# Kernel optimization log

Measured on AMD Instinct MI355X. Metric: run time of the kernel, lower is better.

## Reference

```python
import jax, jax.numpy as jnp
import numpy as np

EMBED_DIM = 1024
NUM_HEAD = 16
HEAD_DIM = EMBED_DIM // NUM_HEAD
SCALE = HEAD_DIM ** -0.5
EPS = 1e-6


def setup_inputs() -> dict:
    key = jax.random.key(0)
    ks = jax.random.split(key, 8)
    B, N, K, D = 4, 2048, 2048, EMBED_DIM
    x = jax.random.normal(ks[0], (B, N, D), dtype=jnp.float32)
    ctx = jax.random.normal(ks[1], (B, K, D), dtype=jnp.float32)
    w_std = 0.02
    q_w = jax.random.normal(ks[2], (D, D), dtype=jnp.float32) * w_std  # [in, out]
    q_b = jnp.zeros((D,), dtype=jnp.float32)
    kv_w = jax.random.normal(ks[3], (D, 2 * D), dtype=jnp.float32) * w_std
    kv_b = jnp.zeros((2 * D,), dtype=jnp.float32)
    proj_w = jax.random.normal(ks[4], (D, D), dtype=jnp.float32) * w_std
    proj_b = jnp.zeros((D,), dtype=jnp.float32)
    return {"x": x, "ctx": ctx, "q_w": q_w, "q_b": q_b,
            "kv_w": kv_w, "kv_b": kv_b, "proj_w": proj_w, "proj_b": proj_b}


def rms_norm(t):
    return t * jax.lax.rsqrt(jnp.mean(t * t, axis=-1, keepdims=True) + EPS)


def reference(x, ctx, q_w, q_b, kv_w, kv_b, proj_w, proj_b):
    B, N, D = x.shape
    Kc = ctx.shape[1]
    H, Hd = NUM_HEAD, HEAD_DIM
    ctxn = rms_norm(ctx)
    q = (x @ q_w + q_b).reshape(B, N, H, Hd)                 # bnhd
    kv = (ctxn @ kv_w + kv_b).reshape(B, Kc, 2, H, Hd)
    k, v = kv[:, :, 0], kv[:, :, 1]                          # bkhd
    logits = jnp.einsum('bnhd,bkhd->bhnk', q * SCALE, k)
    logits = jnp.clip(logits, -10.0, 10.0)
    attn = jax.nn.softmax(logits, axis=-1)                   # bhnk
    out = jnp.einsum('bhnk,bkhd->bnhd', attn, v).reshape(B, N, D)
    out = out @ proj_w + proj_b
    return out, attn.mean()
```

## Files before the change

### kernel.cpp

```cpp
#include <hip/hip_runtime.h>
#include <hip/hip_bf16.h>
#include <stdint.h>


typedef __bf16 bf16_t;
typedef __bf16 bf16x8 __attribute__((ext_vector_type(8)));
typedef __bf16 bf16x4 __attribute__((ext_vector_type(4)));
typedef short  s16x4  __attribute__((ext_vector_type(4)));
typedef float  f32x4  __attribute__((ext_vector_type(4)));

#define BB 4
#define NN 2048
#define KC 2048
#define DD 1024
#define NH 16
#define HD 64
#define QSCALE 0.18033688011112042f
#define CLIP2  14.426950408889634f

__device__ __forceinline__ f32x4 mfma_16x16x32(bf16x8 a, bf16x8 b, f32x4 c) {
  return __builtin_amdgcn_mfma_f32_16x16x32_bf16(a, b, c, 0, 0, 0);
}

__device__ __forceinline__ void gl_lds16(const bf16_t* g, bf16_t* l) {
  __builtin_amdgcn_global_load_lds(
      (const __attribute__((address_space(1))) void*)g,
      (__attribute__((address_space(3))) void*)l, 16, 0, 0);
}

__global__ __launch_bounds__(256) void cvt_f32_bf16(const float* __restrict__ in,
                                                    bf16_t* __restrict__ out, int n4) {
  int i = blockIdx.x * 256 + threadIdx.x;
  if (i >= n4) return;
  float4 v = ((const float4*)in)[i];
  bf16x4 o = {(bf16_t)v.x, (bf16_t)v.y, (bf16_t)v.z, (bf16_t)v.w};
  ((bf16x4*)out)[i] = o;
}

__global__ __launch_bounds__(256) void rmsnorm_rows(const float* __restrict__ in,
                                                    bf16_t* __restrict__ out) {
  int row = blockIdx.x, tid = threadIdx.x;
  float4 v = ((const float4*)(in + (size_t)row * DD))[tid];
  float ss = v.x * v.x + v.y * v.y + v.z * v.z + v.w * v.w;
#pragma unroll
  for (int m = 1; m < 64; m <<= 1) ss += __shfl_xor(ss, m);
  __shared__ float wsum[4];
  if ((tid & 63) == 0) wsum[tid >> 6] = ss;
  __syncthreads();
  float total = wsum[0] + wsum[1] + wsum[2] + wsum[3];
  float scale = rsqrtf(total * (1.0f / (float)DD) + 1e-6f);
  bf16x4 o = {(bf16_t)(v.x * scale), (bf16_t)(v.y * scale),
              (bf16_t)(v.z * scale), (bf16_t)(v.w * scale)};
  ((bf16x4*)(out + (size_t)row * DD))[tid] = o;
}

__global__ __launch_bounds__(256) void transpose_w(const float* __restrict__ W,
                                                   bf16_t* __restrict__ WT, int R, int C) {
  __shared__ float tile[32][33];
  int tx = threadIdx.x & 31, ty = threadIdx.x >> 5;
  int r0 = blockIdx.y * 32, c0 = blockIdx.x * 32;
#pragma unroll
  for (int i = 0; i < 4; i++) tile[ty + 8 * i][tx] = W[(size_t)(r0 + ty + 8 * i) * C + c0 + tx];
  __syncthreads();
#pragma unroll
  for (int i = 0; i < 4; i++)
    WT[(size_t)(c0 + ty + 8 * i) * R + r0 + tx] = (bf16_t)tile[tx][ty + 8 * i];
}

template <int OUT_F32>
__global__ __launch_bounds__(256, 2) void gemm_bt(const bf16_t* __restrict__ A,
                                                  const bf16_t* __restrict__ Bt,
                                                  const float* __restrict__ bias,
                                                  void* __restrict__ Cout, int M, int N,
                                                  int Kd, float alpha) {
  __shared__ bf16_t As[128 * 32];
  __shared__ bf16_t Bs[128 * 32];
  int tid = threadIdx.x;
  int w = tid >> 6, lane = tid & 63;
  int quad = lane >> 4, l16 = lane & 15;
  int row0 = blockIdx.y * 128, col0 = blockIdx.x * 128;
  int wm = (w >> 1) * 64, wn = (w & 1) * 64;

  f32x4 acc[4][4];
#pragma unroll
  for (int i = 0; i < 4; i++)
#pragma unroll
    for (int j = 0; j < 4; j++) acc[i][j] = (f32x4){0.f, 0.f, 0.f, 0.f};

  for (int kk = 0; kk < Kd; kk += 32) {
#pragma unroll
    for (int call = 0; call < 2; call++) {
      int c = w * 128 + call * 64 + lane;
      gl_lds16(&A[(size_t)(row0 + (c >> 2)) * Kd + kk + (c & 3) * 8],
               &As[(w * 128 + call * 64) * 8]);
      gl_lds16(&Bt[(size_t)(col0 + (c >> 2)) * Kd + kk + (c & 3) * 8],
               &Bs[(w * 128 + call * 64) * 8]);
    }
    __syncthreads();
    bf16x8 af[4], bfr[4];
#pragma unroll
    for (int mi = 0; mi < 4; mi++)
      af[mi] = *(const bf16x8*)&As[(wm + mi * 16 + l16) * 32 + quad * 8];
#pragma unroll
    for (int ni = 0; ni < 4; ni++)
      bfr[ni] = *(const bf16x8*)&Bs[(wn + ni * 16 + l16) * 32 + quad * 8];
#pragma unroll
    for (int mi = 0; mi < 4; mi++)
#pragma unroll
      for (int ni = 0; ni < 4; ni++) acc[mi][ni] = mfma_16x16x32(af[mi], bfr[ni], acc[mi][ni]);
    __syncthreads();
  }

#pragma unroll
  for (int ni = 0; ni < 4; ni++) {
    int col = col0 + wn + ni * 16 + l16;
    float bv = bias[col];
#pragma unroll
    for (int mi = 0; mi < 4; mi++) {
#pragma unroll
      for (int r = 0; r < 4; r++) {
        int row = row0 + wm + mi * 16 + quad * 4 + r;
        float v = (acc[mi][ni][r] + bv) * alpha;
        if (OUT_F32)
          ((float*)Cout)[(size_t)row * N + col] = v;
        else
          ((bf16_t*)Cout)[(size_t)row * N + col] = (bf16_t)v;
      }
    }
  }
}

__global__ __launch_bounds__(256) void transpose_v(const bf16_t* __restrict__ kvbuf,
                                                   bf16_t* __restrict__ vT) {
  __shared__ bf16_t tile[64][72];
  int bh = blockIdx.y;
  int b = bh >> 4, h = bh & 15;
  int kc0 = blockIdx.x * 64;
  int tid = threadIdx.x;
#pragma unroll
  for (int i = 0; i < 2; i++) {
    int ch = tid + i * 256;
    int key = ch >> 3, cc = ch & 7;
    *(bf16x8*)&tile[key][cc * 8] =
        *(const bf16x8*)&kvbuf[((size_t)b * KC + kc0 + key) * (2 * DD) + DD + h * HD + cc * 8];
  }
  __syncthreads();
#pragma unroll
  for (int i = 0; i < 2; i++) {
    int ch = tid + i * 256;
    int hd = ch >> 3, cc = ch & 7;
    bf16x8 v;
#pragma unroll
    for (int e = 0; e < 8; e++) v[e] = tile[cc * 8 + e][hd];
    *(bf16x8*)&vT[((size_t)bh * HD + hd) * KC + kc0 + cc * 8] = v;
  }
}

__global__ __launch_bounds__(256, 2) void flash_attn(const bf16_t* __restrict__ qbuf,
                                                     const bf16_t* __restrict__ kvbuf,
                                                     const bf16_t* __restrict__ vT,
                                                     bf16_t* __restrict__ attn_out) {
  __shared__ bf16_t Ks[64][72];
  __shared__ bf16_t Vs[64][72];
  __shared__ float rsinvS[4][64];

  int tid = threadIdx.x, w = tid >> 6, lane = tid & 63;
  int quad = lane >> 4, l16 = lane & 15;
  int bid = blockIdx.x;
  int xcd = bid & 7, slot = bid >> 3;
  int bh = xcd * 8 + (slot >> 3);
  int qt = slot & 7;
  int b = bh >> 4, h = bh & 15;
  int n0 = qt * 256 + w * 64;

  const bf16_t* kbase = kvbuf + (size_t)b * KC * (2 * DD) + (size_t)h * HD;
  const bf16_t* vbase = vT + (size_t)bh * HD * KC;

  bf16x8 qf[4][2];
#pragma unroll
  for (int qi = 0; qi < 4; qi++)
#pragma unroll
    for (int dc = 0; dc < 2; dc++)
      qf[qi][dc] = *(const bf16x8*)&qbuf[((size_t)b * NN + n0 + qi * 16 + l16) * DD + h * HD +
                                         dc * 32 + quad * 8];

  f32x4 o[4][4];
#pragma unroll
  for (int qi = 0; qi < 4; qi++)
#pragma unroll
    for (int hb = 0; hb < 4; hb++) o[qi][hb] = (f32x4){0.f, 0.f, 0.f, 0.f};
  float rs[4] = {0.f, 0.f, 0.f, 0.f};

  for (int kc0 = 0; kc0 < KC; kc0 += 64) {
    __syncthreads();
#pragma unroll
    for (int i = 0; i < 2; i++) {
      int idx = tid + i * 256;
      int r = idx >> 3, c = idx & 7;
      *(bf16x8*)&Ks[r][c * 8] = *(const bf16x8*)&kbase[(size_t)(kc0 + r) * (2 * DD) + c * 8];
      *(bf16x8*)&Vs[r][c * 8] = *(const bf16x8*)&vbase[(size_t)r * KC + kc0 + c * 8];
    }
    __syncthreads();

    bf16x8 kf[4][2];
#pragma unroll
    for (int ki = 0; ki < 4; ki++)
#pragma unroll
      for (int dc = 0; dc < 2; dc++)
        kf[ki][dc] = *(const bf16x8*)&Ks[ki * 16 + l16][dc * 32 + quad * 8];
    union vu_t { bf16x8 v8; s16x4 h[2]; };
    vu_t vb[2][4];
#pragma unroll
    for (int g = 0; g < 2; g++)
#pragma unroll
      for (int hb = 0; hb < 4; hb++) {
        vb[g][hb].h[0] = *(const s16x4*)&Vs[hb * 16 + l16][g * 32 + quad * 4];
        vb[g][hb].h[1] = *(const s16x4*)&Vs[hb * 16 + l16][g * 32 + quad * 4 + 16];
      }

#pragma unroll
    for (int qi = 0; qi < 4; qi++) {
#pragma unroll
      for (int g = 0; g < 2; g++) {
        union { bf16x8 v8; bf16x4 h[2]; } pf;
#pragma unroll
        for (int sub = 0; sub < 2; sub++) {
          f32x4 s = (f32x4){0.f, 0.f, 0.f, 0.f};
          s = mfma_16x16x32(kf[g * 2 + sub][0], qf[qi][0], s);
          s = mfma_16x16x32(kf[g * 2 + sub][1], qf[qi][1], s);
          bf16x4 pb;
#pragma unroll
          for (int r = 0; r < 4; r++) {
            float pv = __builtin_amdgcn_exp2f(__builtin_amdgcn_fmed3f(s[r], -CLIP2, CLIP2));
            rs[qi] += pv;
            pb[r] = (bf16_t)pv;
          }
          pf.h[sub] = pb;
        }
#pragma unroll
        for (int hb = 0; hb < 4; hb++)
          o[qi][hb] = mfma_16x16x32(pf.v8, vb[g][hb].v8, o[qi][hb]);
      }
    }
  }

#pragma unroll
  for (int qi = 0; qi < 4; qi++) {
    float v = rs[qi];
    v += __shfl_xor(v, 16);
    v += __shfl_xor(v, 32);
    if (quad == 0) rsinvS[w][qi * 16 + l16] = 1.0f / v;
  }
#pragma unroll
  for (int qi = 0; qi < 4; qi++) {
    f32x4 ri = *(const f32x4*)&rsinvS[w][qi * 16 + quad * 4];
#pragma unroll
    for (int hb = 0; hb < 4; hb++) {
#pragma unroll
      for (int r = 0; r < 4; r++) {
        int row = n0 + qi * 16 + quad * 4 + r;
        int col = h * HD + hb * 16 + l16;
        attn_out[((size_t)b * NN + row) * DD + col] = (bf16_t)(o[qi][hb][r] * ri[r]);
      }
    }
  }
}

__global__ void write_mean(float* out) { out[0] = 1.0f / 2048.0f; }

extern "C" void kernel_launch(void* const* d_in, const int* in_sizes, int n_in, void* d_out,
                              int out_size, void* d_ws, size_t ws_size, hipStream_t stream) {
  const float* x      = (const float*)d_in[0];
  const float* ctx    = (const float*)d_in[1];
  const float* q_w    = (const float*)d_in[2];
  const float* q_b    = (const float*)d_in[3];
  const float* kv_w   = (const float*)d_in[4];
  const float* kv_b   = (const float*)d_in[5];
  const float* proj_w = (const float*)d_in[6];
  const float* proj_b = (const float*)d_in[7];
  float* out = (float*)d_out;
  char* ws = (char*)d_ws;

  bf16_t* xb    = (bf16_t*)(ws + 0);
  bf16_t* ctxn  = (bf16_t*)(ws + 16777216);
  bf16_t* qwT   = (bf16_t*)(ws + 33554432);
  bf16_t* kvwT  = (bf16_t*)(ws + 35651584);
  bf16_t* pwT   = (bf16_t*)(ws + 39845888);
  bf16_t* qbuf  = (bf16_t*)(ws + 41943040);
  bf16_t* kvbuf = (bf16_t*)(ws + 58720256);
  bf16_t* vT       = ctxn;
  bf16_t* attn_out = xb;

  cvt_f32_bf16<<<8192, 256, 0, stream>>>(x, xb, (BB * NN * DD) / 4);
  rmsnorm_rows<<<BB * KC, 256, 0, stream>>>(ctx, ctxn);
  transpose_w<<<dim3(32, 32), 256, 0, stream>>>(q_w, qwT, DD, DD);
  transpose_w<<<dim3(64, 32), 256, 0, stream>>>(kv_w, kvwT, DD, 2 * DD);
  transpose_w<<<dim3(32, 32), 256, 0, stream>>>(proj_w, pwT, DD, DD);
  gemm_bt<0><<<dim3(8, 64), 256, 0, stream>>>(xb, qwT, q_b, qbuf, BB * NN, DD, DD, QSCALE);
  gemm_bt<0><<<dim3(16, 64), 256, 0, stream>>>(ctxn, kvwT, kv_b, kvbuf, BB * KC, 2 * DD, DD, 1.0f);
  transpose_v<<<dim3(KC / 64, BB * NH), 256, 0, stream>>>(kvbuf, vT);
  flash_attn<<<512, 256, 0, stream>>>(qbuf, kvbuf, vT, attn_out);
  gemm_bt<1><<<dim3(8, 64), 256, 0, stream>>>(attn_out, pwT, proj_b, out, BB * NN, DD, DD, 1.0f);
  write_mean<<<1, 1, 0, stream>>>(out + (size_t)out_size - 1);
}
```

Measured before the change: 330.4 us.

## Pre-pack V into MFMA fragment layout, shrink attention blocks, XCD-aware GEMM tiling

The V transpose kernel now writes V already packed in per-tile MFMA operand order, so flash attention can stream it into LDS with direct global-to-LDS copies and read each fragment with one 16-byte LDS load. Flash attention blocks shrink from 4 waves to 2 waves (128 query rows) with 1024 blocks and launch bounds allowing 4 blocks per CU, aiming for more occupancy and parallelism. The GEMMs switch to a 1D grid remapped so that blocks sharing row panels land on the same XCD, improving L2 reuse. The cost is that each attention block now loads K and V tiles for half as many queries, doubling that load traffic.

```diff
diff --git a/kernel.cpp b/kernel.cpp
--- a/kernel.cpp
+++ b/kernel.cpp
@@ -72,13 +72,16 @@
                                                   const bf16_t* __restrict__ Bt,
                                                   const float* __restrict__ bias,
                                                   void* __restrict__ Cout, int M, int N,
-                                                  int Kd, float alpha) {
+                                                  int Kd, float alpha, int gxlog) {
   __shared__ bf16_t As[128 * 32];
   __shared__ bf16_t Bs[128 * 32];
   int tid = threadIdx.x;
   int w = tid >> 6, lane = tid & 63;
   int quad = lane >> 4, l16 = lane & 15;
-  int row0 = blockIdx.y * 128, col0 = blockIdx.x * 128;
+  int bid = blockIdx.x;
+  int xcd = bid & 7, idx = bid >> 3;
+  int row0 = (xcd * 8 + (idx >> gxlog)) * 128;
+  int col0 = (idx & ((1 << gxlog) - 1)) * 128;
   int wm = (w >> 1) * 64, wn = (w & 1) * 64;
 
   f32x4 acc[4][4];
@@ -131,11 +134,12 @@
 }
 
 __global__ __launch_bounds__(256) void transpose_v(const bf16_t* __restrict__ kvbuf,
-                                                   bf16_t* __restrict__ vT) {
+                                                   bf16_t* __restrict__ vP) {
   __shared__ bf16_t tile[64][72];
   int bh = blockIdx.y;
   int b = bh >> 4, h = bh & 15;
-  int kc0 = blockIdx.x * 64;
+  int t = blockIdx.x;
+  int kc0 = t * 64;
   int tid = threadIdx.x;
 #pragma unroll
   for (int i = 0; i < 2; i++) {
@@ -147,34 +151,35 @@
   __syncthreads();
 #pragma unroll
   for (int i = 0; i < 2; i++) {
-    int ch = tid + i * 256;
-    int hd = ch >> 3, cc = ch & 7;
+    int c = tid + i * 256;
+    int g = c >> 8, hb = (c >> 6) & 3, l16 = (c >> 2) & 15, quad = c & 3;
     bf16x8 v;
 #pragma unroll
-    for (int e = 0; e < 8; e++) v[e] = tile[cc * 8 + e][hd];
-    *(bf16x8*)&vT[((size_t)bh * HD + hd) * KC + kc0 + cc * 8] = v;
-  }
-}
-
-__global__ __launch_bounds__(256, 2) void flash_attn(const bf16_t* __restrict__ qbuf,
+    for (int j = 0; j < 8; j++)
+      v[j] = tile[g * 32 + quad * 4 + (j & 3) + (j >> 2) * 16][hb * 16 + l16];
+    *(bf16x8*)&vP[((size_t)bh * 32 + t) * 4096 + c * 8] = v;
+  }
+}
+
+__global__ __launch_bounds__(128, 4) void flash_attn(const bf16_t* __restrict__ qbuf,
                                                      const bf16_t* __restrict__ kvbuf,
-                                                     const bf16_t* __restrict__ vT,
+                                                     const bf16_t* __restrict__ vP,
                                                      bf16_t* __restrict__ attn_out) {
   __shared__ bf16_t Ks[64][72];
-  __shared__ bf16_t Vs[64][72];
-  __shared__ float rsinvS[4][64];
+  __shared__ bf16_t Vp[4096];
+  __shared__ float rsinvS[2][64];
 
   int tid = threadIdx.x, w = tid >> 6, lane = tid & 63;
   int quad = lane >> 4, l16 = lane & 15;
   int bid = blockIdx.x;
   int xcd = bid & 7, slot = bid >> 3;
-  int bh = xcd * 8 + (slot >> 3);
-  int qt = slot & 7;
+  int bh = xcd * 8 + (slot >> 4);
+  int qt = slot & 15;
   int b = bh >> 4, h = bh & 15;
-  int n0 = qt * 256 + w * 64;
+  int n0 = qt * 128 + w * 64;
 
   const bf16_t* kbase = kvbuf + (size_t)b * KC * (2 * DD) + (size_t)h * HD;
-  const bf16_t* vbase = vT + (size_t)bh * HD * KC;
+  const bf16_t* vpb = vP + (size_t)bh * 32 * 4096;
 
   bf16x8 qf[4][2];
 #pragma unroll
@@ -191,14 +196,19 @@
     for (int hb = 0; hb < 4; hb++) o[qi][hb] = (f32x4){0.f, 0.f, 0.f, 0.f};
   float rs[4] = {0.f, 0.f, 0.f, 0.f};
 
-  for (int kc0 = 0; kc0 < KC; kc0 += 64) {
+  for (int t = 0; t < KC / 64; t++) {
+    int kc0 = t * 64;
     __syncthreads();
 #pragma unroll
-    for (int i = 0; i < 2; i++) {
-      int idx = tid + i * 256;
+    for (int i = 0; i < 4; i++) {
+      int idx = tid + i * 128;
       int r = idx >> 3, c = idx & 7;
       *(bf16x8*)&Ks[r][c * 8] = *(const bf16x8*)&kbase[(size_t)(kc0 + r) * (2 * DD) + c * 8];
-      *(bf16x8*)&Vs[r][c * 8] = *(const bf16x8*)&vbase[(size_t)r * KC + kc0 + c * 8];
+    }
+#pragma unroll
+    for (int i = 0; i < 4; i++) {
+      int j = w * 4 + i;
+      gl_lds16(&vpb[(size_t)t * 4096 + j * 512 + lane * 8], &Vp[j * 512]);
     }
     __syncthreads();
 
@@ -208,15 +218,12 @@
 #pragma unroll
       for (int dc = 0; dc < 2; dc++)
         kf[ki][dc] = *(const bf16x8*)&Ks[ki * 16 + l16][dc * 32 + quad * 8];
-    union vu_t { bf16x8 v8; s16x4 h[2]; };
-    vu_t vb[2][4];
+    bf16x8 vb[2][4];
 #pragma unroll
     for (int g = 0; g < 2; g++)
 #pragma unroll
-      for (int hb = 0; hb < 4; hb++) {
-        vb[g][hb].h[0] = *(const s16x4*)&Vs[hb * 16 + l16][g * 32 + quad * 4];
-        vb[g][hb].h[1] = *(const s16x4*)&Vs[hb * 16 + l16][g * 32 + quad * 4 + 16];
-      }
+      for (int hb = 0; hb < 4; hb++)
+        vb[g][hb] = *(const bf16x8*)&Vp[(g * 4 + hb) * 512 + l16 * 32 + quad * 8];
 
 #pragma unroll
     for (int qi = 0; qi < 4; qi++) {
@@ -239,7 +246,7 @@
         }
 #pragma unroll
         for (int hb = 0; hb < 4; hb++)
-          o[qi][hb] = mfma_16x16x32(pf.v8, vb[g][hb].v8, o[qi][hb]);
+          o[qi][hb] = mfma_16x16x32(pf.v8, vb[g][hb], o[qi][hb]);
       }
     }
   }
@@ -288,7 +295,7 @@
   bf16_t* pwT   = (bf16_t*)(ws + 39845888);
   bf16_t* qbuf  = (bf16_t*)(ws + 41943040);
   bf16_t* kvbuf = (bf16_t*)(ws + 58720256);
-  bf16_t* vT       = ctxn;
+  bf16_t* vP       = ctxn;
   bf16_t* attn_out = xb;
 
   cvt_f32_bf16<<<8192, 256, 0, stream>>>(x, xb, (BB * NN * DD) / 4);
@@ -296,10 +303,10 @@
   transpose_w<<<dim3(32, 32), 256, 0, stream>>>(q_w, qwT, DD, DD);
   transpose_w<<<dim3(64, 32), 256, 0, stream>>>(kv_w, kvwT, DD, 2 * DD);
   transpose_w<<<dim3(32, 32), 256, 0, stream>>>(proj_w, pwT, DD, DD);
-  gemm_bt<0><<<dim3(8, 64), 256, 0, stream>>>(xb, qwT, q_b, qbuf, BB * NN, DD, DD, QSCALE);
-  gemm_bt<0><<<dim3(16, 64), 256, 0, stream>>>(ctxn, kvwT, kv_b, kvbuf, BB * KC, 2 * DD, DD, 1.0f);
-  transpose_v<<<dim3(KC / 64, BB * NH), 256, 0, stream>>>(kvbuf, vT);
-  flash_attn<<<512, 256, 0, stream>>>(qbuf, kvbuf, vT, attn_out);
-  gemm_bt<1><<<dim3(8, 64), 256, 0, stream>>>(attn_out, pwT, proj_b, out, BB * NN, DD, DD, 1.0f);
+  gemm_bt<0><<<512, 256, 0, stream>>>(xb, qwT, q_b, qbuf, BB * NN, DD, DD, QSCALE, 3);
+  gemm_bt<0><<<1024, 256, 0, stream>>>(ctxn, kvwT, kv_b, kvbuf, BB * KC, 2 * DD, DD, 1.0f, 4);
+  transpose_v<<<dim3(KC / 64, BB * NH), 256, 0, stream>>>(kvbuf, vP);
+  flash_attn<<<1024, 128, 0, stream>>>(qbuf, kvbuf, vP, attn_out);
+  gemm_bt<1><<<512, 256, 0, stream>>>(attn_out, pwT, proj_b, out, BB * NN, DD, DD, 1.0f, 3);
   write_mean<<<1, 1, 0, stream>>>(out + (size_t)out_size - 1);
 }
```

After: 807.8 us. +144.5%, slower.
